# Kernel optimization log

Hardware: AMD Instinct MI355X
Metric: run time of the kernel (lower is better)

## Reference

```python
import math
import jax, jax.numpy as jnp
import numpy as np

N_EMBD = 256
N_HEAD = 4
MLP_MULT = 64
N = MLP_MULT * N_EMBD // N_HEAD  # 4096, head feature dim
THETA = 2 ** 16
B, T = 2, 2048


def get_freqs(n: int, theta: int) -> jnp.ndarray:
    # quantize arange to multiples of 2 (pairs share a frequency)
    idx = jnp.arange(n, dtype=jnp.float32)
    q = jnp.floor(idx / 2.0) * 2.0
    return 1.0 / theta ** (q / n) / (2.0 * math.pi)


def _rope(phases: jnp.ndarray, v: jnp.ndarray) -> jnp.ndarray:
    # interleaved rotation: (-v_odd, v_even) re-interleaved
    v_rot = jnp.stack((-v[..., 1::2], v[..., ::2]), axis=-1).reshape(v.shape)
    ph = (phases % 1.0) * (2.0 * math.pi)
    return v * jnp.cos(ph) + v_rot * jnp.sin(ph)


def setup_inputs() -> dict:
    key = jax.random.key(0)
    kq, kk, kv = jax.random.split(key, 3)
    Q = jax.random.normal(kq, (B, N_HEAD, T, N), dtype=jnp.float32)
    K = jax.random.normal(kk, (B, N_HEAD, T, N), dtype=jnp.float32)
    V = jax.random.normal(kv, (B, N_HEAD, T, N), dtype=jnp.float32)
    return {"Q": Q, "K": K, "V": V}


def reference(Q, K, V):
    t = Q.shape[2]
    freqs = get_freqs(N, THETA)  # [N]
    # phases: [1,1,T,N]
    r_phases = jnp.arange(t, dtype=jnp.float32)[None, None, :, None] * freqs[None, None, None, :]
    Q32 = Q.astype(jnp.float32)
    V32 = V.astype(jnp.float32)
    QR = _rope(r_phases, Q32)  # [B,nh,T,N]
    scale = 1.0 / math.sqrt(N)
    scores = jnp.einsum('bhtn,bhsn->bhts', QR, QR) * scale  # [B,nh,T,T], no softmax
    out = jnp.einsum('bhts,bhsn->bhtn', scores, V32)
    return out.astype(Q.dtype)
```

## Files before the change

### kernel.cpp

```cpp
#include <hip/hip_runtime.h>
#include <stdint.h>

#define B_  2
#define H_  4
#define T_  2048
#define N_  4096
#define BH  8

#define BM 256
#define BN 256
#define BK 64

#define ROPE_BLOCKS  ((BH * (long)T_ * N_) / (8 * 256))
#define TRANS_BLOCKS ((T_ / 64) * (N_ / 64) * BH)

typedef __attribute__((ext_vector_type(8))) short  short8;
typedef __attribute__((ext_vector_type(4))) float  floatx4;


__device__ __forceinline__ unsigned short f2bf(float x) {
  union { float f; unsigned u; } un; un.f = x;
  unsigned r = un.u + 0x7FFFu + ((un.u >> 16) & 1u);
  return (unsigned short)(r >> 16);
}

__device__ __forceinline__ void async_copy16(const void* g, void* l) {
  __builtin_amdgcn_global_load_lds(
      (const __attribute__((address_space(1))) unsigned int*)g,
      (__attribute__((address_space(3))) unsigned int*)l,
      16, 0, 0);
}

__global__ __launch_bounds__(256)
void prep_kernel(const float* __restrict__ Q, unsigned short* __restrict__ QR,
                 const float* __restrict__ V, unsigned short* __restrict__ Vt) {
  __shared__ float tile[64][65];
  const int bid = (int)blockIdx.x;

  if (bid < (int)ROPE_BLOCKS) {
    const long e0 = ((long)bid * 256 + threadIdx.x) * 8;
    const float4 v0 = *(const float4*)(Q + e0);
    const float4 v1 = *(const float4*)(Q + e0 + 4);
    const int   n0 = (int)(e0 & (N_ - 1));
    const float t  = (float)((int)((e0 >> 12) & (T_ - 1)));
    float vv[8] = {v0.x, v0.y, v0.z, v0.w, v1.x, v1.y, v1.z, v1.w};
    union { short8 v; unsigned short u[8]; } o;
#pragma unroll
    for (int p = 0; p < 4; ++p) {
      const int n = n0 + 2 * p;
      const float freq = exp2f(-(float)n * (1.0f / 256.0f)) * 0.15915494309189535f;
      const float ph = t * freq;
      const float fr = ph - floorf(ph);
      const float s = __builtin_amdgcn_sinf(fr);
      const float c = __builtin_amdgcn_cosf(fr);
      o.u[2 * p]     = f2bf(vv[2 * p] * c - vv[2 * p + 1] * s);
      o.u[2 * p + 1] = f2bf(vv[2 * p + 1] * c + vv[2 * p] * s);
    }
    *(short8*)(QR + e0) = o.v;
  } else {
    const int tb = bid - (int)ROPE_BLOCKS;
    const int sxi = tb & 31;
    const int nyi = (tb >> 5) & 63;
    const long bh = tb >> 11;
    const float* Vb = V + bh * (long)T_ * N_;
    unsigned short* Vtb = Vt + bh * (long)N_ * T_;
    const int s0 = sxi * 64;
    const int n0 = nyi * 64;
    const int c = threadIdx.x & 15;
    const int r = threadIdx.x >> 4;
#pragma unroll
    for (int i = 0; i < 4; ++i) {
      const float4 v = *(const float4*)(Vb + (long)(s0 + r + 16 * i) * N_ + n0 + c * 4);
      tile[r + 16 * i][c * 4 + 0] = v.x;
      tile[r + 16 * i][c * 4 + 1] = v.y;
      tile[r + 16 * i][c * 4 + 2] = v.z;
      tile[r + 16 * i][c * 4 + 3] = v.w;
    }
    __syncthreads();
    const int rn = threadIdx.x >> 3;
    const int cs = threadIdx.x & 7;
#pragma unroll
    for (int i = 0; i < 2; ++i) {
      const int n = rn + 32 * i;
      union { short8 v; unsigned short u[8]; } o;
#pragma unroll
      for (int k = 0; k < 8; ++k) o.u[k] = f2bf(tile[cs * 8 + k][n]);
      *(short8*)(Vtb + (long)(n0 + n) * T_ + s0 + cs * 8) = o.v;
    }
  }
}

template<int QI, int QJ>
__device__ __forceinline__ void mfma_quad(floatx4 (&acc)[8][4], const short8* a, const short8* b) {
#pragma unroll
  for (int s = 0; s < 2; ++s)
#pragma unroll
    for (int f = 0; f < 4; ++f)
#pragma unroll
      for (int c = 0; c < 2; ++c)
        acc[QI * 4 + f][QJ * 2 + c] = __builtin_amdgcn_mfma_f32_16x16x32_bf16(
            a[f * 2 + s], b[c * 2 + s], acc[QI * 4 + f][QJ * 2 + c], 0, 0, 0);
}

template <typename OutT>
__global__ __launch_bounds__(512, 2)
void gemm_bt8(const unsigned short* __restrict__ A, const unsigned short* __restrict__ B,
              OutT* __restrict__ C, int M, int Nc, int K, float alpha,
              long sA, long sB, long sC)
{
  __shared__ unsigned short smem[4][16384];
  char* smemb = (char*)smem;

  const int nx = (int)gridDim.x, ny = (int)gridDim.y;
  const int nwg = nx * ny * (int)gridDim.z;
  const int idx = (int)blockIdx.x + nx * ((int)blockIdx.y + ny * (int)blockIdx.z);
  const int wg = ((nwg & 7) == 0) ? ((idx & 7) * (nwg >> 3) + (idx >> 3)) : idx;
  const int bx = wg % nx;
  const int by = (wg / nx) % ny;
  const int bz = wg / (nx * ny);

  const unsigned short* Ab = A + bz * sA;
  const unsigned short* Bb = B + bz * sB;
  OutT* Cb = C + bz * sC;
  const int tM = by * BM, tN = bx * BN;

  const int tid  = (int)threadIdx.x;
  const int lane = tid & 63;
  const int wave = tid >> 6;
  const int wm = wave >> 2;
  const int wn = wave & 3;
  const int lr = lane & 15;
  const int lk = (lane >> 4) * 8;

  const unsigned swz   = (unsigned)(lane & 7) << 4;
  const unsigned lowA0 = ((unsigned)(lk * 2)     ) ^ swz;
  const unsigned lowA1 = ((unsigned)(lk * 2) + 64) ^ swz;
  const unsigned aB4   = (unsigned)wm * 16384u + (unsigned)lr * 128u;
  const unsigned bB4   = 32768u + (unsigned)(wn >> 1) * 16384u
                       + (unsigned)(wn & 1) * 8192u + (unsigned)lr * 128u;

  const int sr = wave * 8 + (lane >> 3);
  const int sc = ((((lane & 7) * 16) ^ ((lane >> 3) << 4)) >> 1);
  const unsigned short* gA = Ab + (long)(tM + sr) * K + sc;
  const unsigned short* gB = Bb + (long)(tN + sr) * K + sc;
  const int NT = K / BK;

  #define STAGE2(gbase, kt, h, ldst) do {                                          \
    const unsigned short* _g = (gbase) + (long)(kt) * 64 + (long)((h) * 128) * K;  \
    async_copy16(_g,                (char*)(ldst) + wave * 1024);                  \
    async_copy16(_g + (long)64 * K, (char*)(ldst) + 8192 + wave * 1024);           \
  } while (0)

  STAGE2(gB, 0, 0, smemb + 32768);
  STAGE2(gB, 0, 1, smemb + 32768 + 16384);
  STAGE2(gA, 0, 0, smemb + 0);
  STAGE2(gA, 0, 1, smemb + 16384);
  const int k1 = (NT > 1) ? 1 : 0;
  STAGE2(gB, k1, 0, smemb + 65536 + 32768);
  STAGE2(gB, k1, 1, smemb + 65536 + 32768 + 16384);
  asm volatile("s_waitcnt vmcnt(4)" ::: "memory");
  __builtin_amdgcn_s_barrier();

  floatx4 acc[8][4] = {};
  short8 a[8], b0[4], b1[4];

  for (int t = 0; t < NT; ++t) {
    const unsigned par  = (unsigned)(t & 1) << 16;
    const unsigned parn = par ^ 0x10000u;
    const char* pa0 = smemb + (par + aB4 + lowA0);
    const char* pa1 = smemb + (par + aB4 + lowA1);
    const char* pb0 = smemb + (par + bB4 + lowA0);
    const char* pb1 = smemb + (par + bB4 + lowA1);
    const int ktA = (t + 1 < NT) ? t + 1 : NT - 1;
    const int ktB = (t + 2 < NT) ? t + 2 : NT - 1;

#pragma unroll
    for (int f = 0; f < 4; ++f) {
      a[f * 2 + 0] = *(const short8*)(pa0 + f * 2048);
      a[f * 2 + 1] = *(const short8*)(pa1 + f * 2048);
    }
#pragma unroll
    for (int c = 0; c < 2; ++c) {
      b0[c * 2 + 0] = *(const short8*)(pb0 + c * 2048);
      b0[c * 2 + 1] = *(const short8*)(pb1 + c * 2048);
    }
    STAGE2(gA, ktA, 0, smemb + parn);
    __builtin_amdgcn_s_barrier();
    asm volatile("s_waitcnt lgkmcnt(0)" ::: "memory");
    __builtin_amdgcn_s_setprio(1);
    mfma_quad<0, 0>(acc, a, b0);
    __builtin_amdgcn_s_setprio(0);
    __builtin_amdgcn_s_barrier();

#pragma unroll
    for (int c = 0; c < 2; ++c) {
      b1[c * 2 + 0] = *(const short8*)(pb0 + 4096 + c * 2048);
      b1[c * 2 + 1] = *(const short8*)(pb1 + 4096 + c * 2048);
    }
    STAGE2(gA, ktA, 1, smemb + parn + 16384);
    __builtin_amdgcn_s_barrier();
    asm volatile("s_waitcnt lgkmcnt(0)" ::: "memory");
    __builtin_amdgcn_s_setprio(1);
    mfma_quad<0, 1>(acc, a, b1);
    __builtin_amdgcn_s_setprio(0);
    __builtin_amdgcn_s_barrier();

#pragma unroll
    for (int f = 0; f < 4; ++f) {
      a[f * 2 + 0] = *(const short8*)(pa0 + 8192 + f * 2048);
      a[f * 2 + 1] = *(const short8*)(pa1 + 8192 + f * 2048);
    }
    STAGE2(gB, ktB, 0, smemb + par + 32768);
    __builtin_amdgcn_s_barrier();
    asm volatile("s_waitcnt lgkmcnt(0)" ::: "memory");
    __builtin_amdgcn_s_setprio(1);
    mfma_quad<1, 1>(acc, a, b1);
    __builtin_amdgcn_s_setprio(0);
    __builtin_amdgcn_s_barrier();

    STAGE2(gB, ktB, 1, smemb + par + 32768 + 16384);
    asm volatile("s_waitcnt vmcnt(4)" ::: "memory");
    __builtin_amdgcn_s_barrier();
    __builtin_amdgcn_s_setprio(1);
    mfma_quad<1, 0>(acc, a, b0);
    __builtin_amdgcn_s_setprio(0);
    __builtin_amdgcn_s_barrier();
  }
  #undef STAGE2

  const int crow = (lane >> 4) * 4;
  const int ccol = lane & 15;
#pragma unroll
  for (int f = 0; f < 8; ++f)
#pragma unroll
    for (int c = 0; c < 4; ++c)
#pragma unroll
      for (int r = 0; r < 4; ++r) {
        const long row = tM + wm * 128 + f * 16 + crow + r;
        const long col = tN + wn * 64 + c * 16 + ccol;
        const float v = acc[f][c][r] * alpha;
        OutT* p = &Cb[row * (long)Nc + col];
        if constexpr (sizeof(OutT) == 2) *p = (OutT)f2bf(v);
        else                             *p = (OutT)v;
      }
}

extern "C" void kernel_launch(void* const* d_in, const int* in_sizes, int n_in,
                              void* d_out, int out_size, void* d_ws, size_t ws_size,
                              hipStream_t stream) {
  const float* Q = (const float*)d_in[0];
  const float* V = (const float*)d_in[2];
  float* O = (float*)d_out;

  unsigned short* QRb = (unsigned short*)d_ws;
  unsigned short* Vtb = QRb + (size_t)BH * T_ * N_;
  unsigned short* S   = Vtb + (size_t)BH * T_ * N_;

  prep_kernel<<<(int)(ROPE_BLOCKS + TRANS_BLOCKS), 256, 0, stream>>>(Q, QRb, V, Vtb);
  gemm_bt8<unsigned short><<<dim3(T_ / BN, T_ / BM, BH), 512, 0, stream>>>(
      QRb, QRb, S, T_, T_, N_, 1.0f / 64.0f,
      (long)T_ * N_, (long)T_ * N_, (long)T_ * T_);
  gemm_bt8<float><<<dim3(N_ / BN, T_ / BM, BH), 512, 0, stream>>>(
      S, Vtb, O, T_, N_, T_, 1.0f,
      (long)T_ * T_, (long)N_ * T_, (long)T_ * N_);
}
```

Before: 1.151 ms.

## Software-pipeline LDS fragment loads behind MFMA quads in GEMM main loop

Restructures the GEMM inner loop so the register fragments for the next MFMA quad are read from LDS while the current quad runs, with a prologue loading the first fragments. The quad order changes to (0,0),(0,1),(1,0),(1,1) so the next tile's A/B fragments can be prefetched at the end of each iteration. Barriers are cut and the vmcnt wait is moved. The goal is to hide LDS read latency behind matrix instructions, at the cost of more register pressure and tighter reasoning about double-buffer hazards.

```diff
diff --git a/kernel.cpp b/kernel.cpp
--- a/kernel.cpp
+++ b/kernel.cpp
@@ -164,66 +164,89 @@
   floatx4 acc[8][4] = {};
   short8 a[8], b0[4], b1[4];
 
+  {
+    const char* pa0 = smemb + (aB4 + lowA0);
+    const char* pa1 = smemb + (aB4 + lowA1);
+    const char* pb0 = smemb + (bB4 + lowA0);
+    const char* pb1 = smemb + (bB4 + lowA1);
+#pragma unroll
+    for (int f = 0; f < 4; ++f) {
+      a[f * 2 + 0] = *(const short8*)(pa0 + f * 2048);
+      a[f * 2 + 1] = *(const short8*)(pa1 + f * 2048);
+    }
+#pragma unroll
+    for (int c = 0; c < 2; ++c) {
+      b0[c * 2 + 0] = *(const short8*)(pb0 + c * 2048);
+      b0[c * 2 + 1] = *(const short8*)(pb1 + c * 2048);
+    }
+  }
+
   for (int t = 0; t < NT; ++t) {
     const unsigned par  = (unsigned)(t & 1) << 16;
     const unsigned parn = par ^ 0x10000u;
-    const char* pa0 = smemb + (par + aB4 + lowA0);
-    const char* pa1 = smemb + (par + aB4 + lowA1);
-    const char* pb0 = smemb + (par + bB4 + lowA0);
-    const char* pb1 = smemb + (par + bB4 + lowA1);
+    const char* pa0c = smemb + (par + aB4 + lowA0);
+    const char* pa1c = smemb + (par + aB4 + lowA1);
+    const char* pb0c = smemb + (par + bB4 + lowA0);
+    const char* pb1c = smemb + (par + bB4 + lowA1);
+    const char* pa0n = smemb + (parn + aB4 + lowA0);
+    const char* pa1n = smemb + (parn + aB4 + lowA1);
+    const char* pb0n = smemb + (parn + bB4 + lowA0);
+    const char* pb1n = smemb + (parn + bB4 + lowA1);
     const int ktA = (t + 1 < NT) ? t + 1 : NT - 1;
     const int ktB = (t + 2 < NT) ? t + 2 : NT - 1;
 
+    STAGE2(gA, ktA, 0, smemb + parn);
+    __builtin_amdgcn_s_setprio(1);
+    mfma_quad<0, 0>(acc, a, b0);
+    __builtin_amdgcn_s_setprio(0);
+    __builtin_amdgcn_sched_barrier(0);
+#pragma unroll
+    for (int c = 0; c < 2; ++c) {
+      b1[c * 2 + 0] = *(const short8*)(pb0c + 4096 + c * 2048);
+      b1[c * 2 + 1] = *(const short8*)(pb1c + 4096 + c * 2048);
+    }
+    asm volatile("s_waitcnt lgkmcnt(0)" ::: "memory");
+    __builtin_amdgcn_s_barrier();
+
+    STAGE2(gA, ktA, 1, smemb + parn + 16384);
+    __builtin_amdgcn_s_setprio(1);
+    mfma_quad<0, 1>(acc, a, b1);
+    __builtin_amdgcn_s_setprio(0);
+    __builtin_amdgcn_sched_barrier(0);
 #pragma unroll
     for (int f = 0; f < 4; ++f) {
-      a[f * 2 + 0] = *(const short8*)(pa0 + f * 2048);
-      a[f * 2 + 1] = *(const short8*)(pa1 + f * 2048);
-    }
+      a[f * 2 + 0] = *(const short8*)(pa0c + 8192 + f * 2048);
+      a[f * 2 + 1] = *(const short8*)(pa1c + 8192 + f * 2048);
+    }
+    asm volatile("s_waitcnt lgkmcnt(0)" ::: "memory");
+    __builtin_amdgcn_s_barrier();
+
+    STAGE2(gB, ktB, 0, smemb + par + 32768);
+    asm volatile("s_waitcnt vmcnt(2)" ::: "memory");
+    __builtin_amdgcn_s_barrier();
+    __builtin_amdgcn_s_setprio(1);
+    mfma_quad<1, 0>(acc, a, b0);
+    __builtin_amdgcn_s_setprio(0);
+    __builtin_amdgcn_sched_barrier(0);
 #pragma unroll
     for (int c = 0; c < 2; ++c) {
-      b0[c * 2 + 0] = *(const short8*)(pb0 + c * 2048);
-      b0[c * 2 + 1] = *(const short8*)(pb1 + c * 2048);
-    }
-    STAGE2(gA, ktA, 0, smemb + parn);
-    __builtin_amdgcn_s_barrier();
-    asm volatile("s_waitcnt lgkmcnt(0)" ::: "memory");
-    __builtin_amdgcn_s_setprio(1);
-    mfma_quad<0, 0>(acc, a, b0);
-    __builtin_amdgcn_s_setprio(0);
-    __builtin_amdgcn_s_barrier();
-
-#pragma unroll
-    for (int c = 0; c < 2; ++c) {
-      b1[c * 2 + 0] = *(const short8*)(pb0 + 4096 + c * 2048);
-      b1[c * 2 + 1] = *(const short8*)(pb1 + 4096 + c * 2048);
-    }
-    STAGE2(gA, ktA, 1, smemb + parn + 16384);
-    __builtin_amdgcn_s_barrier();
-    asm volatile("s_waitcnt lgkmcnt(0)" ::: "memory");
-    __builtin_amdgcn_s_setprio(1);
-    mfma_quad<0, 1>(acc, a, b1);
-    __builtin_amdgcn_s_setprio(0);
-    __builtin_amdgcn_s_barrier();
-
+      b0[c * 2 + 0] = *(const short8*)(pb0n + c * 2048);
+      b0[c * 2 + 1] = *(const short8*)(pb1n + c * 2048);
+    }
+    asm volatile("s_waitcnt lgkmcnt(0)" ::: "memory");
+    __builtin_amdgcn_s_barrier();
+
+    STAGE2(gB, ktB, 1, smemb + par + 32768 + 16384);
+    __builtin_amdgcn_s_setprio(1);
+    mfma_quad<1, 1>(acc, a, b1);
+    __builtin_amdgcn_s_setprio(0);
+    __builtin_amdgcn_sched_barrier(0);
 #pragma unroll
     for (int f = 0; f < 4; ++f) {
-      a[f * 2 + 0] = *(const short8*)(pa0 + 8192 + f * 2048);
-      a[f * 2 + 1] = *(const short8*)(pa1 + 8192 + f * 2048);
-    }
-    STAGE2(gB, ktB, 0, smemb + par + 32768);
-    __builtin_amdgcn_s_barrier();
-    asm volatile("s_waitcnt lgkmcnt(0)" ::: "memory");
-    __builtin_amdgcn_s_setprio(1);
-    mfma_quad<1, 1>(acc, a, b1);
-    __builtin_amdgcn_s_setprio(0);
-    __builtin_amdgcn_s_barrier();
-
-    STAGE2(gB, ktB, 1, smemb + par + 32768 + 16384);
-    asm volatile("s_waitcnt vmcnt(4)" ::: "memory");
-    __builtin_amdgcn_s_barrier();
-    __builtin_amdgcn_s_setprio(1);
-    mfma_quad<1, 0>(acc, a, b0);
-    __builtin_amdgcn_s_setprio(0);
+      a[f * 2 + 0] = *(const short8*)(pa0n + f * 2048);
+      a[f * 2 + 1] = *(const short8*)(pa1n + f * 2048);
+    }
+    asm volatile("s_waitcnt lgkmcnt(0)" ::: "memory");
     __builtin_amdgcn_s_barrier();
   }
   #undef STAGE2
```

Measured after the change: 1.174 ms. Within noise of the previous version (+2.0%).
